# Kernel optimization log

Hardware: AMD Instinct MI355X
Metric: run time of the kernel (lower is better)

## Reference

```python
import jax, jax.numpy as jnp
import numpy as np

B, S, D_IN, D_OUT, H = 4, 2048, 1024, 1024, 16
HD = D_OUT // H


def setup_inputs() -> dict:
    key = jax.random.key(0)
    ks = jax.random.split(key, 6)
    s_in = 1.0 / np.sqrt(D_IN)
    s_out = 1.0 / np.sqrt(D_OUT)
    return {
        "x": jax.random.normal(ks[0], (B, S, D_IN), dtype=jnp.float32),
        "W_q": jax.random.uniform(ks[1], (D_OUT, D_IN), jnp.float32, -s_in, s_in),
        "W_k": jax.random.uniform(ks[2], (D_OUT, D_IN), jnp.float32, -s_in, s_in),
        "W_v": jax.random.uniform(ks[3], (D_OUT, D_IN), jnp.float32, -s_in, s_in),
        "W_o": jax.random.uniform(ks[4], (D_OUT, D_OUT), jnp.float32, -s_out, s_out),
        "b_o": jax.random.uniform(ks[5], (D_OUT,), jnp.float32, -s_out, s_out),
    }


def reference(x, W_q, W_k, W_v, W_o, b_o):
    b, s, _ = x.shape
    # torch Linear: y = x @ W.T  (no qkv bias)
    q = (x @ W_q.T).reshape(b, s, H, HD).transpose(0, 2, 1, 3)  # [b,h,s,hd]
    k = (x @ W_k.T).reshape(b, s, H, HD).transpose(0, 2, 1, 3)
    v = (x @ W_v.T).reshape(b, s, H, HD).transpose(0, 2, 1, 3)
    scores = jnp.einsum("bhqd,bhkd->bhqk", q, k)  # [b,h,s,s]
    causal = jnp.triu(jnp.ones((s, s), dtype=bool), k=1)
    scores = jnp.where(causal, -jnp.inf, scores)
    attn = jax.nn.softmax(scores / np.sqrt(HD), axis=-1)
    # dropout p=0.0 -> identity
    ctx = jnp.einsum("bhqk,bhkd->bhqd", attn, v)  # [b,h,s,hd]
    ctx = ctx.transpose(0, 2, 1, 3).reshape(b, s, D_OUT)
    return ctx @ W_o.T + b_o
```

## Files before the change

### kernel.cpp

```cpp
#include <hip/hip_runtime.h>
#include <cstdint>
#include <cstddef>

#define S_LEN  2048
#define NHEAD  16
#define HDIM   64
#define KD     1024
#define BSROWS 8192

typedef __attribute__((ext_vector_type(4))) float          floatx4;
typedef __attribute__((ext_vector_type(8))) __bf16         bf16x8;
typedef __attribute__((ext_vector_type(8))) unsigned short ushort8v;
typedef __attribute__((ext_vector_type(4))) unsigned short ushort4v;
typedef __attribute__((ext_vector_type(4))) float          float4v;

__device__ __forceinline__ unsigned short f2bf(float f) {
  unsigned int u = __float_as_uint(f);
  u += 0x7fffu + ((u >> 16) & 1u);
  return (unsigned short)(u >> 16);
}

#if __has_builtin(__builtin_amdgcn_exp2f)
#define EXP2F(x) __builtin_amdgcn_exp2f(x)
#else
#define EXP2F(x) exp2f(x)
#endif

__device__ __forceinline__ unsigned int pack2bf(float a, float b) {
#if __has_builtin(__builtin_amdgcn_perm)
  return __builtin_amdgcn_perm(__float_as_uint(b), __float_as_uint(a), 0x07060302);
#else
  return (__float_as_uint(a) >> 16) | (__float_as_uint(b) & 0xffff0000u);
#endif
}

__device__ __forceinline__ void async_cp16(const void* gsrc, void* ldst) {
  __builtin_amdgcn_global_load_lds(
      (__attribute__((address_space(1))) void*)gsrc,
      (__attribute__((address_space(3))) void*)ldst,
      16, 0, 0);
}

#define XN4 2097152
#define WN4 262144

__global__ __launch_bounds__(256) void cvt_kernel(
    const float* __restrict__ x,  const float* __restrict__ wq,
    const float* __restrict__ wk, const float* __restrict__ wv,
    const float* __restrict__ wo,
    unsigned short* __restrict__ xb, unsigned short* __restrict__ wqkvb,
    unsigned short* __restrict__ wob)
{
  const int i = blockIdx.x * 256 + threadIdx.x;
  const float* src; unsigned short* dst; int off;
  if (i < XN4) { src = x; dst = xb; off = i; }
  else {
    const int j = i - XN4;
    if (j < WN4)          { src = wq; dst = wqkvb;           off = j; }
    else if (j < 2*WN4)   { src = wk; dst = wqkvb + 4*WN4;   off = j - WN4; }
    else if (j < 3*WN4)   { src = wv; dst = wqkvb + 8*WN4;   off = j - 2*WN4; }
    else                  { src = wo; dst = wob;             off = j - 3*WN4; }
  }
  const float4v v = ((const float4v*)src)[off];
  ushort4v o;
  o.x = f2bf(v.x); o.y = f2bf(v.y); o.z = f2bf(v.z); o.w = f2bf(v.w);
  ((ushort4v*)dst)[off] = o;
}

__device__ __forceinline__ void stage_h12(
    const int h, const int tk,
    const unsigned short* __restrict__ gAs,
    const unsigned short* __restrict__ gBs,
    unsigned short* smem, const int wave)
{
  const int bufo = (tk & 1) * 24576;
  const unsigned short* g;
  unsigned short* l;
  if (h == 0)      { g = gAs + tk * 64;                      l = smem + bufo + wave * 512; }
  else if (h == 1) { g = gBs + tk * 64;                      l = smem + bufo + 8192  + wave * 512; }
  else             { g = gBs + (size_t)128 * KD + tk * 64;   l = smem + bufo + 16384 + wave * 512; }
  async_cp16(g,                   l);
  async_cp16(g + (size_t)64 * KD, l + 4096);
}

template<bool SWAP>
__device__ __forceinline__ void kloop12(
    const unsigned short* __restrict__ gAs,
    const unsigned short* __restrict__ gBs,
    unsigned short* smem, floatx4 (&acc)[4][4],
    const int wave, const int quad, const int l15)
{
  const int ar_base = (wave >> 2) * 64 + l15;
  const int bc_base = (wave & 3) * 64 + l15;
  const int sw0 = ((quad)     ^ (l15 & 7)) * 8;
  const int sw1 = ((4 + quad) ^ (l15 & 7)) * 8;

  bf16x8 af[4][2];
  bf16x8 bfr[2][2];

  stage_h12(0, 0, gAs, gBs, smem, wave);
  stage_h12(1, 0, gAs, gBs, smem, wave);
  stage_h12(2, 0, gAs, gBs, smem, wave);

#define MFMAQ12(nh)                                                            \
  __builtin_amdgcn_s_setprio(1);                                               \
  _Pragma("unroll") for (int mt = 0; mt < 4; ++mt)                             \
    _Pragma("unroll") for (int nt = 0; nt < 2; ++nt)                           \
      _Pragma("unroll") for (int ks = 0; ks < 2; ++ks) {                       \
        if (SWAP)                                                              \
          acc[mt][(nh)*2+nt] = __builtin_amdgcn_mfma_f32_16x16x32_bf16(        \
              bfr[nt][ks], af[mt][ks], acc[mt][(nh)*2+nt], 0, 0, 0);           \
        else                                                                   \
          acc[mt][(nh)*2+nt] = __builtin_amdgcn_mfma_f32_16x16x32_bf16(        \
              af[mt][ks], bfr[nt][ks], acc[mt][(nh)*2+nt], 0, 0, 0);           \
      }                                                                        \
  __builtin_amdgcn_s_setprio(0);

#pragma unroll 2
  for (int t = 0; t < 16; ++t) {
    const unsigned short* As = smem + (t & 1) * 24576;
    const unsigned short* Bs = As + 8192;

    asm volatile("s_barrier" ::: "memory");
    if (t + 1 < 16) {
      stage_h12(0, t + 1, gAs, gBs, smem, wave);
      stage_h12(1, t + 1, gAs, gBs, smem, wave);
    }
    if (t < 15) asm volatile("s_waitcnt vmcnt(4)\n\ts_barrier" ::: "memory");
    else        asm volatile("s_waitcnt vmcnt(0)\n\ts_barrier" ::: "memory");
#pragma unroll
    for (int mt = 0; mt < 4; ++mt) {
      const unsigned short* ar = &As[(ar_base + mt * 16) * 64];
      af[mt][0] = *(const bf16x8*)(ar + sw0);
      af[mt][1] = *(const bf16x8*)(ar + sw1);
    }
#pragma unroll
    for (int nt = 0; nt < 2; ++nt) {
      const unsigned short* br = &Bs[(bc_base + nt * 16) * 64];
      bfr[nt][0] = *(const bf16x8*)(br + sw0);
      bfr[nt][1] = *(const bf16x8*)(br + sw1);
    }
    MFMAQ12(0)

    asm volatile("s_barrier" ::: "memory");
    if (t + 1 < 16) stage_h12(2, t + 1, gAs, gBs, smem, wave);
#pragma unroll
    for (int nt = 0; nt < 2; ++nt) {
      const unsigned short* br = &Bs[(bc_base + 32 + nt * 16) * 64];
      bfr[nt][0] = *(const bf16x8*)(br + sw0);
      bfr[nt][1] = *(const bf16x8*)(br + sw1);
    }
    MFMAQ12(1)
  }
#undef MFMAQ12
}

__global__ __launch_bounds__(512, 2) void gemm_qkv12(
    const unsigned short* __restrict__ A,
    const unsigned short* __restrict__ Bw,
    unsigned short* __restrict__ Qo,
    unsigned short* __restrict__ Ko,
    unsigned short* __restrict__ Vto)
{
  __shared__ unsigned short smem[49152];
  const int tid  = threadIdx.x;
  const int wave = tid >> 6, lane = tid & 63;
  const int quad = lane >> 4, l15 = lane & 15;

  const int bid = (int)blockIdx.x;
  const int tau = (bid & 7) * 96 + (bid >> 3);
  const int m0 = (tau / 12) * 128, n0 = (tau % 12) * 256;

  const int strow = tid >> 3;
  const int stxc  = (tid & 7) ^ (strow & 7);
  const unsigned short* gAs = A  + (size_t)(m0 + strow) * KD + stxc * 8;
  const unsigned short* gBs = Bw + (size_t)(n0 + strow) * KD + stxc * 8;

  const floatx4 fzero = {0.f, 0.f, 0.f, 0.f};
  floatx4 acc[4][4];
#pragma unroll
  for (int i = 0; i < 4; i++)
#pragma unroll
    for (int j = 0; j < 4; j++) acc[i][j] = fzero;

  const int which = n0 >> 10;
  if (which < 2) kloop12<true >(gAs, gBs, smem, acc, wave, quad, l15);
  else           kloop12<false>(gAs, gBs, smem, acc, wave, quad, l15);

  const int h0 = (n0 & 1023) >> 6;
  const int b = m0 >> 11, sl = m0 & 2047;
  __syncthreads();

  if (which < 2) {
    unsigned short* dst = which ? Ko : Qo;
    const float scale = which ? 1.0f : 0.18033688011112042f;
#pragma unroll
    for (int mt = 0; mt < 4; ++mt)
#pragma unroll
      for (int jn = 0; jn < 4; ++jn) {
        ushort4v t4;
#pragma unroll
        for (int r = 0; r < 4; ++r) t4[r] = f2bf(acc[mt][jn][r] * scale);
        const int row = (wave >> 2) * 64 + mt * 16 + l15;
        const int col = (wave & 3) * 64 + (jn >> 1) * 32 + (jn & 1) * 16 + quad * 4;
        *(ushort4v*)&smem[row * 264 + col] = t4;
      }
    __syncthreads();
#pragma unroll
    for (int t8 = 0; t8 < 8; ++t8) {
      const int c = t8 * 512 + tid;
      const int sr = c >> 5, ch = c & 31;
      const int hs = ch >> 3, hd8 = (ch & 7) * 8;
      const ushort8v val = *(const ushort8v*)&smem[sr * 264 + hs * 64 + hd8];
      *(ushort8v*)&dst[((size_t)((b * NHEAD + h0 + hs) * S_LEN + sl + sr)) * HDIM + hd8] = val;
    }
  } else {
#pragma unroll
    for (int mt = 0; mt < 4; ++mt)
#pragma unroll
      for (int jn = 0; jn < 4; ++jn) {
        ushort4v t4;
#pragma unroll
        for (int r = 0; r < 4; ++r) t4[r] = f2bf(acc[mt][jn][r]);
        const int nl = (wave & 3) * 64 + (jn >> 1) * 32 + (jn & 1) * 16 + l15;
        const int sc = (wave >> 2) * 64 + mt * 16 + quad * 4;
        *(ushort4v*)&smem[nl * 136 + sc] = t4;
      }
    __syncthreads();
#pragma unroll
    for (int t8 = 0; t8 < 8; ++t8) {
      const int c = t8 * 512 + tid;
      const int nl = c >> 4, sc8 = (c & 15) * 8;
      const ushort8v val = *(const ushort8v*)&smem[nl * 136 + sc8];
      *(ushort8v*)&Vto[((size_t)((b * NHEAD + h0 + (nl >> 6)) * HDIM + (nl & 63))) * S_LEN + sl + sc8] = val;
    }
  }
}

template<bool SWAP>
__device__ __forceinline__ void kloop128(
    const unsigned short* __restrict__ gA,
    const unsigned short* __restrict__ gB,
    unsigned short* smem, floatx4 (&acc)[4][4],
    const int wave, const int quad, const int l15,
    const int wr, const int wc)
{
  {
    unsigned short* lA = smem + wave * 1024;
    unsigned short* lB = smem + 4096 + wave * 1024;
    async_cp16(gA,                    lA);
    async_cp16(gA + (size_t)16 * KD,  lA + 512);
    async_cp16(gB,                    lB);
    async_cp16(gB + (size_t)16 * KD,  lB + 512);
  }
  const int lsw = (l15 >> 1) & 3;

#pragma unroll 2
  for (int it = 0; it < 32; it++) {
    asm volatile("s_waitcnt vmcnt(0) lgkmcnt(0)\n\ts_barrier" ::: "memory");
    if (it + 1 < 32) {
      const int nb = (it + 1) & 1;
      const int ko = (it + 1) * 32;
      unsigned short* lA = smem + nb * 8192 + wave * 1024;
      unsigned short* lB = smem + nb * 8192 + 4096 + wave * 1024;
      async_cp16(gA + ko,                   lA);
      async_cp16(gA + ko + (size_t)16 * KD, lA + 512);
      async_cp16(gB + ko,                   lB);
      async_cp16(gB + ko + (size_t)16 * KD, lB + 512);
    }
    const unsigned short* As = smem + (it & 1) * 8192;
    const unsigned short* Bs = As + 4096;

    bf16x8 af[4], bfrag[4];
#pragma unroll
    for (int i = 0; i < 4; i++)
      af[i] = *(const bf16x8*)&As[(wr * 64 + i * 16 + l15) * 32 + (quad ^ lsw) * 8];
#pragma unroll
    for (int j = 0; j < 4; j++)
      bfrag[j] = *(const bf16x8*)&Bs[(wc * 64 + j * 16 + l15) * 32 + (quad ^ lsw) * 8];
#pragma unroll
    for (int i = 0; i < 4; i++)
#pragma unroll
      for (int j = 0; j < 4; j++) {
        if (SWAP)
          acc[i][j] = __builtin_amdgcn_mfma_f32_16x16x32_bf16(bfrag[j], af[i], acc[i][j], 0, 0, 0);
        else
          acc[i][j] = __builtin_amdgcn_mfma_f32_16x16x32_bf16(af[i], bfrag[j], acc[i][j], 0, 0, 0);
      }
  }
}

__global__ __launch_bounds__(512, 6) void attn_kernel(
    const unsigned short* __restrict__ Qg_,
    const unsigned short* __restrict__ Kg_,
    const unsigned short* __restrict__ Vtg_,
    unsigned short* __restrict__ CTX)
{
  __shared__ unsigned short smem[25088];
  const int tid  = threadIdx.x, wave = tid >> 6, lane = tid & 63;
  const int quad = lane >> 4, l15 = lane & 15;
  unsigned short* Pw = smem + 16384 + wave * 1088;

  const int bh = (int)blockIdx.x;
  const int yy = (int)blockIdx.y;
  const int qt = (yy < 4) ? yy : (yy < 8) ? (11 - yy) : (yy < 12) ? yy : (27 - yy);
  const int q0 = qt * 128;
  const size_t base = (size_t)bh * (S_LEN * HDIM);
  const unsigned short* Qg  = Qg_  + base;
  const unsigned short* Kg  = Kg_  + base;
  const unsigned short* Vtg = Vtg_ + base;
  const int qw = q0 + wave * 16;

  const int strow = lane >> 3;
  const int stxc  = (lane & 7) ^ strow;
  const unsigned short* kstage = Kg  + (size_t)(wave * 8 + strow) * HDIM  + stxc * 8;
  const unsigned short* vstage = Vtg + (size_t)(wave * 8 + strow) * S_LEN + stxc * 8;
  unsigned short* kd0 = smem + wave * 512;
  unsigned short* vd0 = smem + 4096 + wave * 512;

  async_cp16(kstage, kd0);
  async_cp16(vstage, vd0);

  bf16x8 qf[2];
#pragma unroll
  for (int ks = 0; ks < 2; ks++)
    qf[ks] = *(const bf16x8*)&Qg[(size_t)(qw + l15) * HDIM + ks * 32 + quad * 8];

  const int sw0 = ((quad)     ^ (l15 & 7)) * 8;
  const int sw1 = ((4 + quad) ^ (l15 & 7)) * 8;

  const floatx4 fzero = {0.f, 0.f, 0.f, 0.f};
  floatx4 O[4];
  float l_part = 0.f;
#pragma unroll
  for (int mt = 0; mt < 4; mt++) O[mt] = fzero;

  const int ntiles = 2 * qt + 2;

  for (int j = 0; j < ntiles; j++) {
    asm volatile("s_waitcnt vmcnt(0) lgkmcnt(0)\n\ts_barrier" ::: "memory");
    if (j + 1 < ntiles) {
      const int nb = (j + 1) & 1;
      async_cp16(kstage + (size_t)(j + 1) * 64 * HDIM, kd0 + nb * 8192);
      async_cp16(vstage + (size_t)(j + 1) * 64,        vd0 + nb * 8192);
    }
    const int k0 = j * 64;
    if (k0 > qw + 15) continue;
    const unsigned short* Ksb = smem + (j & 1) * 8192;
    const unsigned short* Vsb = Ksb + 4096;
    const int krel = qw + 15 - k0;

    floatx4 sa[4];
#pragma unroll
    for (int kt = 0; kt < 4; kt++) sa[kt] = fzero;
    __builtin_amdgcn_s_setprio(1);
#pragma unroll
    for (int kt = 0; kt < 4; kt++) {
      if (kt * 16 <= krel) {
        const unsigned short* kr = &Ksb[(kt * 16 + l15) * 64];
        sa[kt] = __builtin_amdgcn_mfma_f32_16x16x32_bf16(*(const bf16x8*)(kr + sw0), qf[0], sa[kt], 0, 0, 0);
        sa[kt] = __builtin_amdgcn_mfma_f32_16x16x32_bf16(*(const bf16x8*)(kr + sw1), qf[1], sa[kt], 0, 0, 0);
      }
    }
    __builtin_amdgcn_s_setprio(0);

    const int qrow = qw + l15;
#pragma unroll
    for (int kt = 0; kt < 4; kt++) {
      const int kbase = k0 + kt * 16;
      unsigned short* pdst = &Pw[l15 * 68 + kt * 16 + quad * 4];
      if (kt * 16 <= krel) {
        if (kbase + 15 > qw) {
#pragma unroll
          for (int r = 0; r < 4; r++)
            if (kbase + quad * 4 + r > qrow) sa[kt][r] = -INFINITY;
        }
        const float p0 = EXP2F(sa[kt][0]), p1 = EXP2F(sa[kt][1]);
        const float p2 = EXP2F(sa[kt][2]), p3 = EXP2F(sa[kt][3]);
        l_part += (p0 + p1) + (p2 + p3);
        uint2 pk; pk.x = pack2bf(p0, p1); pk.y = pack2bf(p2, p3);
        *(uint2*)pdst = pk;
      } else if ((kt >> 1) * 32 <= krel) {
        uint2 z; z.x = 0u; z.y = 0u;
        *(uint2*)pdst = z;
      }
    }
    asm volatile("s_waitcnt lgkmcnt(0)" ::: "memory");

#pragma unroll
    for (int ks = 0; ks < 2; ks++) {
      if (ks * 32 > krel) break;
      const unsigned short* ps = &Pw[l15 * 68 + ks * 32 + quad * 8];
      union { ushort4v h[2]; bf16x8 v; } pu;
      pu.h[0] = *(const ushort4v*)ps;
      pu.h[1] = *(const ushort4v*)(ps + 4);
      __builtin_amdgcn_s_setprio(1);
#pragma unroll
      for (int mt = 0; mt < 4; mt++) {
        const bf16x8 vf = *(const bf16x8*)(&Vsb[(mt * 16 + l15) * 64] + (ks ? sw1 : sw0));
        O[mt] = __builtin_amdgcn_mfma_f32_16x16x32_bf16(vf, pu.v, O[mt], 0, 0, 0);
      }
      __builtin_amdgcn_s_setprio(0);
    }
  }

#pragma unroll
  for (int d = 16; d < 64; d <<= 1)
    l_part += __shfl_xor(l_part, d, 64);

  {
    const float inv = 1.0f / l_part;
#pragma unroll
    for (int mt = 0; mt < 4; mt++)
#pragma unroll
      for (int a = 0; a < 2; a++) {
        const unsigned int pk =
            (unsigned int)f2bf(O[mt][2 * a] * inv) |
            ((unsigned int)f2bf(O[mt][2 * a + 1] * inv) << 16);
        *(unsigned int*)&Pw[l15 * 68 + mt * 16 + quad * 4 + 2 * a] = pk;
      }
  }
  asm volatile("s_waitcnt lgkmcnt(0)" ::: "memory");
  const int b = bh >> 4, h = bh & 15;
#pragma unroll
  for (int it = 0; it < 2; it++) {
    const int g = it * 64 + lane;
    const int row = g >> 3, c8 = (g & 7) * 8;
    union { ushort4v h[2]; ushort8v v; } ou;
    ou.h[0] = *(const ushort4v*)&Pw[row * 68 + c8];
    ou.h[1] = *(const ushort4v*)&Pw[row * 68 + c8 + 4];
    const int s = qw + row;
    *(ushort8v*)&CTX[((size_t)(b * S_LEN + s)) * KD + h * HDIM + c8] = ou.v;
  }
}

__global__ __launch_bounds__(256) void gemm_out(
    const unsigned short* __restrict__ A,
    const unsigned short* __restrict__ Bw,
    const float* __restrict__ bias,
    float* __restrict__ out)
{
  __shared__ unsigned short smem[16384];
  const int tid  = threadIdx.x;
  const int wave = tid >> 6, lane = tid & 63;
  const int quad = lane >> 4, l15 = lane & 15;
  const int wr = wave >> 1, wc = wave & 1;
  const int m0 = blockIdx.x * 128, n0 = blockIdx.y * 128;

  const int srow = lane >> 2;
  const int scol = ((lane & 3) ^ ((srow >> 1) & 3)) * 8;
  const unsigned short* gA = A  + (size_t)(m0 + wave * 32 + srow) * KD + scol;
  const unsigned short* gB = Bw + (size_t)(n0 + wave * 32 + srow) * KD + scol;

  const floatx4 fzero = {0.f, 0.f, 0.f, 0.f};
  floatx4 acc[4][4];
#pragma unroll
  for (int i = 0; i < 4; i++)
#pragma unroll
    for (int j = 0; j < 4; j++) acc[i][j] = fzero;

  kloop128<true>(gA, gB, smem, acc, wave, quad, l15, wr, wc);

#pragma unroll
  for (int j = 0; j < 4; j++) {
    const int nb4 = n0 + wc * 64 + j * 16 + quad * 4;
    const float4v bb = *(const float4v*)&bias[nb4];
#pragma unroll
    for (int i = 0; i < 4; i++) {
      const int m = m0 + wr * 64 + i * 16 + l15;
      float4v st;
#pragma unroll
      for (int r = 0; r < 4; r++) st[r] = acc[i][j][r] + bb[r];
      *(float4v*)&out[(size_t)m * KD + nb4] = st;
    }
  }
}

extern "C" void kernel_launch(void* const* d_in, const int* in_sizes, int n_in,
                              void* d_out, int out_size, void* d_ws, size_t ws_size,
                              hipStream_t stream) {
  (void)in_sizes; (void)n_in; (void)out_size;
  const float* x  = (const float*)d_in[0];
  const float* wq = (const float*)d_in[1];
  const float* wk = (const float*)d_in[2];
  const float* wv = (const float*)d_in[3];
  const float* wo = (const float*)d_in[4];
  const float* bo = (const float*)d_in[5];
  float* out = (float*)d_out;

  if (ws_size < (size_t)92274688) return;
  char* ws = (char*)d_ws;
  unsigned short* xb    = (unsigned short*)(ws);
  unsigned short* wqkvb = (unsigned short*)(ws + (size_t)16777216);
  unsigned short* wob   = (unsigned short*)(ws + (size_t)23068672);
  unsigned short* qws   = (unsigned short*)(ws + (size_t)25165824);
  unsigned short* kws   = (unsigned short*)(ws + (size_t)41943040);
  unsigned short* vtws  = (unsigned short*)(ws + (size_t)58720256);
  unsigned short* ctxws = (unsigned short*)(ws + (size_t)75497472);

  cvt_kernel<<<12288, 256, 0, stream>>>(x, wq, wk, wv, wo, xb, wqkvb, wob);
  gemm_qkv12<<<768, 512, 0, stream>>>(xb, wqkvb, qws, kws, vtws);
  attn_kernel<<<dim3(64, 16), 512, 0, stream>>>(qws, kws, vtws, ctxws);
  gemm_out<<<dim3(64, 8), 256, 0, stream>>>(ctxws, wob, bo, out);
}
```

Measured before the change: 239.2 us.

## Reuse QKV GEMM k-loop for output projection with 128x256 tiles

```diff
diff --git a/kernel.cpp b/kernel.cpp
--- a/kernel.cpp
+++ b/kernel.cpp
@@ -237,59 +237,6 @@
   }
 }
 
-template<bool SWAP>
-__device__ __forceinline__ void kloop128(
-    const unsigned short* __restrict__ gA,
-    const unsigned short* __restrict__ gB,
-    unsigned short* smem, floatx4 (&acc)[4][4],
-    const int wave, const int quad, const int l15,
-    const int wr, const int wc)
-{
-  {
-    unsigned short* lA = smem + wave * 1024;
-    unsigned short* lB = smem + 4096 + wave * 1024;
-    async_cp16(gA,                    lA);
-    async_cp16(gA + (size_t)16 * KD,  lA + 512);
-    async_cp16(gB,                    lB);
-    async_cp16(gB + (size_t)16 * KD,  lB + 512);
-  }
-  const int lsw = (l15 >> 1) & 3;
-
-#pragma unroll 2
-  for (int it = 0; it < 32; it++) {
-    asm volatile("s_waitcnt vmcnt(0) lgkmcnt(0)\n\ts_barrier" ::: "memory");
-    if (it + 1 < 32) {
-      const int nb = (it + 1) & 1;
-      const int ko = (it + 1) * 32;
-      unsigned short* lA = smem + nb * 8192 + wave * 1024;
-      unsigned short* lB = smem + nb * 8192 + 4096 + wave * 1024;
-      async_cp16(gA + ko,                   lA);
-      async_cp16(gA + ko + (size_t)16 * KD, lA + 512);
-      async_cp16(gB + ko,                   lB);
-      async_cp16(gB + ko + (size_t)16 * KD, lB + 512);
-    }
-    const unsigned short* As = smem + (it & 1) * 8192;
-    const unsigned short* Bs = As + 4096;
-
-    bf16x8 af[4], bfrag[4];
-#pragma unroll
-    for (int i = 0; i < 4; i++)
-      af[i] = *(const bf16x8*)&As[(wr * 64 + i * 16 + l15) * 32 + (quad ^ lsw) * 8];
-#pragma unroll
-    for (int j = 0; j < 4; j++)
-      bfrag[j] = *(const bf16x8*)&Bs[(wc * 64 + j * 16 + l15) * 32 + (quad ^ lsw) * 8];
-#pragma unroll
-    for (int i = 0; i < 4; i++)
-#pragma unroll
-      for (int j = 0; j < 4; j++) {
-        if (SWAP)
-          acc[i][j] = __builtin_amdgcn_mfma_f32_16x16x32_bf16(bfrag[j], af[i], acc[i][j], 0, 0, 0);
-        else
-          acc[i][j] = __builtin_amdgcn_mfma_f32_16x16x32_bf16(af[i], bfrag[j], acc[i][j], 0, 0, 0);
-      }
-  }
-}
-
 __global__ __launch_bounds__(512, 6) void attn_kernel(
     const unsigned short* __restrict__ Qg_,
     const unsigned short* __restrict__ Kg_,
@@ -434,23 +381,25 @@
   }
 }
 
-__global__ __launch_bounds__(256) void gemm_out(
+__global__ __launch_bounds__(512, 2) void gemm_out12(
     const unsigned short* __restrict__ A,
     const unsigned short* __restrict__ Bw,
     const float* __restrict__ bias,
     float* __restrict__ out)
 {
-  __shared__ unsigned short smem[16384];
+  __shared__ unsigned short smem[49152];
   const int tid  = threadIdx.x;
   const int wave = tid >> 6, lane = tid & 63;
   const int quad = lane >> 4, l15 = lane & 15;
-  const int wr = wave >> 1, wc = wave & 1;
-  const int m0 = blockIdx.x * 128, n0 = blockIdx.y * 128;
-
-  const int srow = lane >> 2;
-  const int scol = ((lane & 3) ^ ((srow >> 1) & 3)) * 8;
-  const unsigned short* gA = A  + (size_t)(m0 + wave * 32 + srow) * KD + scol;
-  const unsigned short* gB = Bw + (size_t)(n0 + wave * 32 + srow) * KD + scol;
+
+  const int bid = (int)blockIdx.x;
+  const int tau = (bid & 7) * 32 + (bid >> 3);
+  const int m0 = (tau >> 2) * 128, n0 = (tau & 3) * 256;
+
+  const int strow = tid >> 3;
+  const int stxc  = (tid & 7) ^ (strow & 7);
+  const unsigned short* gAs = A  + (size_t)(m0 + strow) * KD + stxc * 8;
+  const unsigned short* gBs = Bw + (size_t)(n0 + strow) * KD + stxc * 8;
 
   const floatx4 fzero = {0.f, 0.f, 0.f, 0.f};
   floatx4 acc[4][4];
@@ -459,18 +408,18 @@
 #pragma unroll
     for (int j = 0; j < 4; j++) acc[i][j] = fzero;
 
-  kloop128<true>(gA, gB, smem, acc, wave, quad, l15, wr, wc);
-
-#pragma unroll
-  for (int j = 0; j < 4; j++) {
-    const int nb4 = n0 + wc * 64 + j * 16 + quad * 4;
+  kloop12<true>(gAs, gBs, smem, acc, wave, quad, l15);
+
+#pragma unroll
+  for (int jn = 0; jn < 4; ++jn) {
+    const int nb4 = n0 + (wave & 3) * 64 + (jn >> 1) * 32 + (jn & 1) * 16 + quad * 4;
     const float4v bb = *(const float4v*)&bias[nb4];
 #pragma unroll
-    for (int i = 0; i < 4; i++) {
-      const int m = m0 + wr * 64 + i * 16 + l15;
+    for (int mt = 0; mt < 4; ++mt) {
+      const int m = m0 + (wave >> 2) * 64 + mt * 16 + l15;
       float4v st;
 #pragma unroll
-      for (int r = 0; r < 4; r++) st[r] = acc[i][j][r] + bb[r];
+      for (int r = 0; r < 4; ++r) st[r] = acc[mt][jn][r] + bb[r];
       *(float4v*)&out[(size_t)m * KD + nb4] = st;
     }
   }
@@ -501,5 +450,5 @@
   cvt_kernel<<<12288, 256, 0, stream>>>(x, wq, wk, wv, wo, xb, wqkvb, wob);
   gemm_qkv12<<<768, 512, 0, stream>>>(xb, wqkvb, qws, kws, vtws);
   attn_kernel<<<dim3(64, 16), 512, 0, stream>>>(qws, kws, vtws, ctxws);
-  gemm_out<<<dim3(64, 8), 256, 0, stream>>>(ctxws, wob, bo, out);
-}
+  gemm_out12<<<256, 512, 0, stream>>>(ctxws, wob, bo, out);
+}
```

Measured after the change: 226.0 us. 1.06x faster.
